# Performance work log

Hardware: AMD Instinct MI355X
Metric: run time of the kernel (lower is better)

The kernel has to match this reference:

```python
import jax, jax.numpy as jnp
import numpy as np

B, N, M, C, K = 4, 16384, 512, 256, 24
EPS = 1e-5


def setup_inputs() -> dict:
    key = jax.random.key(0)
    ks = jax.random.split(key, 5)
    return {
        "x": jax.random.normal(ks[0], (B, N, C), jnp.float32),
        "coords": jax.random.normal(ks[1], (B, N, 3), jnp.float32),
        "anchors": jax.random.normal(ks[2], (B, M, 3), jnp.float32),
        "fc_w": jax.random.normal(ks[3], (C, C), jnp.float32) * 0.05,
        "fc_b": jax.random.normal(ks[4], (C,), jnp.float32) * 0.05,
        "bn_gamma": jnp.ones((C,), jnp.float32),
        "bn_beta": jnp.zeros((C,), jnp.float32),
    }


def _build_incidence(coords, anchors):
    # squared distances suffice for top-k ordering (monotone in cdist)
    d2 = (
        jnp.sum(coords * coords, -1)[:, :, None]
        + jnp.sum(anchors * anchors, -1)[:, None, :]
        - 2.0 * jnp.einsum("bnd,bmd->bnm", coords, anchors)
    )  # [B,N,M]
    k = min(K, anchors.shape[1])
    _, idx = jax.lax.top_k(-d2, k)  # [B,N,k] nearest anchors
    b = jnp.arange(coords.shape[0])[:, None, None]
    n = jnp.arange(coords.shape[1])[None, :, None]
    H = jnp.zeros(d2.shape, d2.dtype).at[b, n, idx].set(1.0)
    return jax.lax.stop_gradient(H)  # built under torch.no_grad()


def _hypconv(x, H, fc_w, fc_b):
    xf = x @ fc_w.T + fc_b  # [B,N,C]
    deg_e = jnp.sum(H, axis=1)  # [B,M]  hyperedge degrees
    inv_e = jnp.where(deg_e > 0, 1.0 / deg_e, 0.0)[..., None]
    E = jnp.einsum("bnm,bnc->bmc", H, xf) * inv_e  # v -> e mean agg
    deg_v = jnp.sum(H, axis=2)  # [B,N]  node degrees
    inv_v = jnp.where(deg_v > 0, 1.0 / deg_v, 0.0)[..., None]
    return jnp.einsum("bnm,bmc->bnc", H, E) * inv_v  # e -> v mean agg


def reference(x, coords, anchors, fc_w, fc_b, bn_gamma, bn_beta):
    H = _build_incidence(coords, anchors)
    x = _hypconv(x, H, fc_w, fc_b) + x  # residual, [B,N,C]
    x = jnp.transpose(x, (0, 2, 1))  # [B,C,N]
    # BatchNorm1d (training-mode batch stats) over (B, N) per channel
    mean = jnp.mean(x, axis=(0, 2), keepdims=True)
    var = jnp.var(x, axis=(0, 2), keepdims=True)
    y = (x - mean) * jax.lax.rsqrt(var + EPS)
    y = y * bn_gamma[None, :, None] + bn_beta[None, :, None]
    return y * jax.nn.sigmoid(y)  # SiLU
```

## Files before the change

### kernel.cpp

```cpp
#include <hip/hip_runtime.h>

#define BB 4
#define NN 16384
#define MM 512
#define CCH 256
#define KNN 24
#define EPSV 1e-5f

typedef unsigned short ushort_t;

__device__ __forceinline__ unsigned int pk_bf16(float a, float b) {
    unsigned int ua = __float_as_uint(a), ub = __float_as_uint(b);
    ua += 0x7FFFu + ((ua >> 16) & 1u);
    ub += 0x7FFFu + ((ub >> 16) & 1u);
    return (ua >> 16) | (ub & 0xFFFF0000u);
}
__device__ __forceinline__ float lo_bf(unsigned int u) { return __uint_as_float(u << 16); }
__device__ __forceinline__ float hi_bf(unsigned int u) { return __uint_as_float(u & 0xFFFF0000u); }

__global__ __launch_bounds__(256) void k_cvt(const float* __restrict__ x,
                                             unsigned int* __restrict__ xh) {
    int i = blockIdx.x * 256 + threadIdx.x;
    float2 v = ((const float2*)x)[i];
    xh[i] = pk_bf16(v.x, v.y);
}

__global__ __launch_bounds__(256) void k_wt(const float* __restrict__ W, float* __restrict__ Wt) {
    int i = blockIdx.x * 256 + threadIdx.x;
    int co = i >> 8, ci = i & 255;
    Wt[(ci << 8) + co] = W[i];
}

#define AE(K) "v_max_u32 v89, v88, " K "\n\tv_min_u32 " K ", v88, " K "\n\t"
#define AO(K) "v_max_u32 v88, v89, " K "\n\tv_min_u32 " K ", v89, " K "\n\t"
#define BE(K) "v_max_u32 v91, v90, " K "\n\tv_min_u32 " K ", v90, " K "\n\t"
#define BO(K) "v_max_u32 v90, v91, " K "\n\tv_min_u32 " K ", v91, " K "\n\t"
#define CE(K) "v_max_u32 v93, v92, " K "\n\tv_min_u32 " K ", v92, " K "\n\t"
#define CO(K) "v_max_u32 v92, v93, " K "\n\tv_min_u32 " K ", v93, " K "\n\t"
#define DE(K) "v_max_u32 v95, v94, " K "\n\tv_min_u32 " K ", v94, " K "\n\t"
#define DO_(K) "v_max_u32 v94, v95, " K "\n\tv_min_u32 " K ", v95, " K "\n\t"
#define CHAIN4 \
    AE("v64") \
    AO("v65") BE("v64") \
    AE("v66") BO("v65") CE("v64") \
    AO("v67") BE("v66") CO("v65") DE("v64") \
    AE("v68") BO("v67") CE("v66") DO_("v65") \
    AO("v69") BE("v68") CO("v67") DE("v66") \
    AE("v70") BO("v69") CE("v68") DO_("v67") \
    AO("v71") BE("v70") CO("v69") DE("v68") \
    AE("v72") BO("v71") CE("v70") DO_("v69") \
    AO("v73") BE("v72") CO("v71") DE("v70") \
    AE("v74") BO("v73") CE("v72") DO_("v71") \
    AO("v75") BE("v74") CO("v73") DE("v72") \
    AE("v76") BO("v75") CE("v74") DO_("v73") \
    AO("v77") BE("v76") CO("v75") DE("v74") \
    AE("v78") BO("v77") CE("v76") DO_("v75") \
    AO("v79") BE("v78") CO("v77") DE("v76") \
    AE("v80") BO("v79") CE("v78") DO_("v77") \
    AO("v81") BE("v80") CO("v79") DE("v78") \
    AE("v82") BO("v81") CE("v80") DO_("v79") \
    AO("v83") BE("v82") CO("v81") DE("v80") \
    AE("v84") BO("v83") CE("v82") DO_("v81") \
    AO("v85") BE("v84") CO("v83") DE("v82") \
    AE("v86") BO("v85") CE("v84") DO_("v83") \
    AO("v87") BE("v86") CO("v85") DE("v84") \
              BO("v87") CE("v86") DO_("v85") \
                        CO("v87") DE("v86") \
                                  DO_("v87")
#define MRG(MI, KJ, K23MJ, K12PJ, K11MJ) \
    { unsigned int sA_ = (unsigned int)__shfl_xor((int)(K23MJ), 32); \
      unsigned int sB_ = (unsigned int)__shfl_xor((int)(K12PJ), 32); \
      MI = ((half == 0) ? min((KJ), sA_) : min(sB_, (K11MJ))) & 511u; }
__global__ __launch_bounds__(128, 2) void k_topk(const float* __restrict__ coords,
                                                 const float* __restrict__ anchors,
                                                 ushort_t* __restrict__ idx_out,
                                                 int* __restrict__ histT) {
    __shared__ float4 alds[MM];
    __shared__ int    hist[MM];
    int tid = threadIdx.x;
    int blk = blockIdx.x;
    int b  = blk >> 8;
    int g  = blk & 255;
    int n0 = g << 6;
    int lane = tid & 63;
    int half = lane >> 5;
    int n = n0 + ((tid >> 6) << 5) + (lane & 31);

    for (int m = tid; m < MM; m += 128) {
        float x_ = anchors[(b * MM + m) * 3 + 0];
        float y_ = anchors[(b * MM + m) * 3 + 1];
        float z_ = anchors[(b * MM + m) * 3 + 2];
        alds[m] = make_float4(x_, y_, z_, x_ * x_ + y_ * y_ + z_ * z_);
        hist[m] = 0;
    }
    __syncthreads();

    float cx = coords[(b * NN + n) * 3 + 0];
    float cy = coords[(b * NN + n) * 3 + 1];
    float cz = coords[(b * NN + n) * 3 + 2];
    float cn2 = cx * cx + cy * cy + cz * cz;

    unsigned int k0 = 0xFFFFFFFFu, k1 = 0xFFFFFFFFu, k2 = 0xFFFFFFFFu, k3 = 0xFFFFFFFFu,
                 k4 = 0xFFFFFFFFu, k5 = 0xFFFFFFFFu, k6 = 0xFFFFFFFFu, k7 = 0xFFFFFFFFu,
                 k8 = 0xFFFFFFFFu, k9 = 0xFFFFFFFFu, k10 = 0xFFFFFFFFu, k11 = 0xFFFFFFFFu,
                 k12 = 0xFFFFFFFFu, k13 = 0xFFFFFFFFu, k14 = 0xFFFFFFFFu, k15 = 0xFFFFFFFFu,
                 k16 = 0xFFFFFFFFu, k17 = 0xFFFFFFFFu, k18 = 0xFFFFFFFFu, k19 = 0xFFFFFFFFu,
                 k20 = 0xFFFFFFFFu, k21 = 0xFFFFFFFFu, k22 = 0xFFFFFFFFu, k23 = 0xFFFFFFFFu;

    int base = half << 8;
    float4 a0 = alds[base + 0];
    float4 a1 = alds[base + 1];
    float4 a2 = alds[base + 2];
    float4 a3 = alds[base + 3];
    float4 a4 = alds[base + 4];
    float4 a5 = alds[base + 5];
    float4 a6 = alds[base + 6];
    float4 a7 = alds[base + 7];
    for (int mm = 0; mm < 32; ++mm) {
        int nxt = (8 * mm + 8) & 255;
        float4 p0 = alds[base + nxt + 0];
        float4 p1 = alds[base + nxt + 1];
        float4 p2 = alds[base + nxt + 2];
        float4 p3 = alds[base + nxt + 3];
        float4 p4 = alds[base + nxt + 4];
        float4 p5 = alds[base + nxt + 5];
        float4 p6 = alds[base + nxt + 6];
        float4 p7 = alds[base + nxt + 7];
        float cd0 = cn2 + a0.w - 2.0f * (cx * a0.x + cy * a0.y + cz * a0.z);
        float cd1 = cn2 + a1.w - 2.0f * (cx * a1.x + cy * a1.y + cz * a1.z);
        float cd2 = cn2 + a2.w - 2.0f * (cx * a2.x + cy * a2.y + cz * a2.z);
        float cd3 = cn2 + a3.w - 2.0f * (cx * a3.x + cy * a3.y + cz * a3.z);
        float cd4 = cn2 + a4.w - 2.0f * (cx * a4.x + cy * a4.y + cz * a4.z);
        float cd5 = cn2 + a5.w - 2.0f * (cx * a5.x + cy * a5.y + cz * a5.z);
        float cd6 = cn2 + a6.w - 2.0f * (cx * a6.x + cy * a6.y + cz * a6.z);
        float cd7 = cn2 + a7.w - 2.0f * (cx * a7.x + cy * a7.y + cz * a7.z);
        int id0 = base + 8 * mm;
        unsigned int cA = ((__float_as_uint(cd0) ^ 0x80000000u) & 0xFFFFFE00u) | (unsigned)(id0 + 0);
        unsigned int cB = ((__float_as_uint(cd1) ^ 0x80000000u) & 0xFFFFFE00u) | (unsigned)(id0 + 1);
        unsigned int cC = ((__float_as_uint(cd2) ^ 0x80000000u) & 0xFFFFFE00u) | (unsigned)(id0 + 2);
        unsigned int cD = ((__float_as_uint(cd3) ^ 0x80000000u) & 0xFFFFFE00u) | (unsigned)(id0 + 3);
        unsigned int cE = ((__float_as_uint(cd4) ^ 0x80000000u) & 0xFFFFFE00u) | (unsigned)(id0 + 4);
        unsigned int cF = ((__float_as_uint(cd5) ^ 0x80000000u) & 0xFFFFFE00u) | (unsigned)(id0 + 5);
        unsigned int cG = ((__float_as_uint(cd6) ^ 0x80000000u) & 0xFFFFFE00u) | (unsigned)(id0 + 6);
        unsigned int cH = ((__float_as_uint(cd7) ^ 0x80000000u) & 0xFFFFFE00u) | (unsigned)(id0 + 7);
        asm volatile(
            CHAIN4
            "v_mov_b32 v88, v96\n\t"
            "v_mov_b32 v90, v98\n\t"
            "v_mov_b32 v92, v100\n\t"
            "v_mov_b32 v94, v102\n\t"
            CHAIN4
            : "+{v64}"(k0),  "+{v65}"(k1),  "+{v66}"(k2),  "+{v67}"(k3),
              "+{v68}"(k4),  "+{v69}"(k5),  "+{v70}"(k6),  "+{v71}"(k7),
              "+{v72}"(k8),  "+{v73}"(k9),  "+{v74}"(k10), "+{v75}"(k11),
              "+{v76}"(k12), "+{v77}"(k13), "+{v78}"(k14), "+{v79}"(k15),
              "+{v80}"(k16), "+{v81}"(k17), "+{v82}"(k18), "+{v83}"(k19),
              "+{v84}"(k20), "+{v85}"(k21), "+{v86}"(k22), "+{v87}"(k23),
              "+{v88}"(cA), "+{v90}"(cB), "+{v92}"(cC), "+{v94}"(cD),
              "+{v96}"(cE), "+{v98}"(cF), "+{v100}"(cG), "+{v102}"(cH)
            :
            : "v89", "v91", "v93", "v95");
        a0 = p0; a1 = p1; a2 = p2; a3 = p3;
        a4 = p4; a5 = p5; a6 = p6; a7 = p7;
    }

    unsigned int Mi0, Mi1, Mi2, Mi3, Mi4, Mi5, Mi6, Mi7, Mi8, Mi9, Mi10, Mi11;
    MRG(Mi0,  k0,  k23, k12, k11)
    MRG(Mi1,  k1,  k22, k13, k10)
    MRG(Mi2,  k2,  k21, k14, k9)
    MRG(Mi3,  k3,  k20, k15, k8)
    MRG(Mi4,  k4,  k19, k16, k7)
    MRG(Mi5,  k5,  k18, k17, k6)
    MRG(Mi6,  k6,  k17, k18, k5)
    MRG(Mi7,  k7,  k16, k19, k4)
    MRG(Mi8,  k8,  k15, k20, k3)
    MRG(Mi9,  k9,  k14, k21, k2)
    MRG(Mi10, k10, k13, k22, k1)
    MRG(Mi11, k11, k12, k23, k0)

    atomicAdd(&hist[Mi0], 1);  atomicAdd(&hist[Mi1], 1);
    atomicAdd(&hist[Mi2], 1);  atomicAdd(&hist[Mi3], 1);
    atomicAdd(&hist[Mi4], 1);  atomicAdd(&hist[Mi5], 1);
    atomicAdd(&hist[Mi6], 1);  atomicAdd(&hist[Mi7], 1);
    atomicAdd(&hist[Mi8], 1);  atomicAdd(&hist[Mi9], 1);
    atomicAdd(&hist[Mi10], 1); atomicAdd(&hist[Mi11], 1);

    unsigned int* ob = (unsigned int*)(idx_out + (size_t)(b * NN + n) * KNN + half * 12);
    ob[0] = Mi0 | (Mi1 << 16);
    ob[1] = Mi2 | (Mi3 << 16);
    ob[2] = Mi4 | (Mi5 << 16);
    ob[3] = Mi6 | (Mi7 << 16);
    ob[4] = Mi8 | (Mi9 << 16);
    ob[5] = Mi10 | (Mi11 << 16);

    __syncthreads();
    for (int m = tid; m < MM; m += 128)
        histT[((((b << 9) + m)) << 8) + g] = hist[m];
}

__global__ __launch_bounds__(64) void k_scan(const int* __restrict__ histT,
                                             int* __restrict__ posT,
                                             int* __restrict__ deg) {
    int e = blockIdx.x;
    int t = threadIdx.x;
    int4 v = ((const int4*)(histT + (e << 8)))[t];
    int s = v.x + v.y + v.z + v.w;
    int inc = s;
    #pragma unroll
    for (int off = 1; off < 64; off <<= 1) {
        int u = __shfl_up(inc, off);
        if (t >= off) inc += u;
    }
    int excl = inc - s;
    int4 o;
    o.x = excl; o.y = excl + v.x; o.z = o.y + v.y; o.w = o.z + v.z;
    ((int4*)(posT + (e << 8)))[t] = o;
    if (t == 63) deg[e] = inc;
}

__global__ __launch_bounds__(256) void k_offsets(const int* __restrict__ deg,
                                                 int* __restrict__ offs) {
    __shared__ int part[256];
    int t = threadIdx.x;
    int v[8];
    int s = 0;
    #pragma unroll
    for (int j = 0; j < 8; ++j) { v[j] = deg[t * 8 + j]; s += v[j]; }
    part[t] = s;
    __syncthreads();
    for (int off = 1; off < 256; off <<= 1) {
        int val = (t >= off) ? part[t - off] : 0;
        __syncthreads();
        part[t] += val;
        __syncthreads();
    }
    int excl = part[t] - s;
    #pragma unroll
    for (int j = 0; j < 8; ++j) { offs[t * 8 + j] = excl; excl += v[j]; }
}

__global__ __launch_bounds__(256) void k_fill2(const unsigned int* __restrict__ idxu,
                                               const int* __restrict__ posT,
                                               const int* __restrict__ offs,
                                               ushort_t* __restrict__ list) {
    __shared__ int pos[MM];
    __shared__ unsigned int ebuf[768];
    int tid = threadIdx.x;
    int blk = blockIdx.x;
    int b = blk >> 8, g = blk & 255;
    int n0 = g << 6;

    for (int m = tid; m < MM; m += 256) {
        int e = (b << 9) + m;
        pos[m] = offs[e] + posT[(e << 8) + g];
    }
    for (int i = tid; i < 768; i += 256)
        ebuf[i] = idxu[(size_t)(b * NN + n0) * 12 + i];
    __syncthreads();

    for (int i = tid; i < 768; i += 256) {
        unsigned int u = ebuf[i];
        int node = n0 + (i / 12);
        int p0 = atomicAdd(&pos[u & 0xFFFFu], 1);
        list[p0] = (ushort_t)node;
        int p1 = atomicAdd(&pos[u >> 16], 1);
        list[p1] = (ushort_t)node;
    }
}

__global__ __launch_bounds__(256) void k_edge2a(const unsigned int* __restrict__ xh,
                                                const ushort_t* __restrict__ list,
                                                const int* __restrict__ offs,
                                                const int* __restrict__ deg,
                                                float* __restrict__ S) {
    __shared__ ushort_t nl[256];
    __shared__ float red[8][64];
    int tid = threadIdx.x;
    int bi = blockIdx.x;
    int r = bi >> 12;
    int grp = (bi & 7) | (r << 3);
    int b = grp & 3;
    int q = grp >> 2;
    int e = (b << 9) | ((bi >> 3) & 511);
    int d = deg[e];
    int o = offs[e];
    int cp = tid & 31, rs = tid >> 5;
    const unsigned int* xb = xh + ((size_t)b << 21) + (q << 5);

    float l0 = 0.f, h0 = 0.f, l1 = 0.f, h1 = 0.f;
    for (int base2 = 0; base2 < d; base2 += 256) {
        int cnt = min(256, d - base2);
        if (tid < cnt) nl[tid] = list[(size_t)o + base2 + tid];
        __syncthreads();
        int i = 0;
        for (; i + 15 < cnt; i += 16) {
            unsigned int u0 = xb[((size_t)nl[i + rs] << 7) + cp];
            unsigned int u1 = xb[((size_t)nl[i + 8 + rs] << 7) + cp];
            l0 += lo_bf(u0); h0 += hi_bf(u0);
            l1 += lo_bf(u1); h1 += hi_bf(u1);
        }
        for (; i + 7 < cnt; i += 8) {
            unsigned int u = xb[((size_t)nl[i + rs] << 7) + cp];
            l0 += lo_bf(u); h0 += hi_bf(u);
        }
        if (i + rs < cnt) {
            unsigned int u = xb[((size_t)nl[i + rs] << 7) + cp];
            l1 += lo_bf(u); h1 += hi_bf(u);
        }
        __syncthreads();
    }
    red[rs][2 * cp] = l0 + l1;
    red[rs][2 * cp + 1] = h0 + h1;
    __syncthreads();
    if (tid < 64) {
        float s = 0.f;
        #pragma unroll
        for (int j = 0; j < 8; ++j) s += red[j][tid];
        S[((size_t)e << 8) + (q << 6) + tid] = s;
    }
}

__global__ __launch_bounds__(256) void k_edge2b(const float* __restrict__ S,
                                                const int* __restrict__ deg,
                                                const float* __restrict__ Wt,
                                                const float* __restrict__ fcb,
                                                unsigned int* __restrict__ Eph) {
    __shared__ float srow[CCH];
    __shared__ float rrow[CCH];
    int tid = threadIdx.x;
    int e = blockIdx.x;
    int d = deg[e];
    float inv = (d > 0) ? (1.0f / (float)d) : 0.0f;
    srow[tid] = S[((size_t)e << 8) + tid] * inv;
    __syncthreads();

    float c0 = (d > 0) ? fcb[tid] : 0.0f;
    float c1 = 0.f, c2 = 0.f, c3 = 0.f;
    #pragma unroll 4
    for (int ci = 0; ci < CCH; ci += 4) {
        c0 = fmaf(srow[ci + 0], Wt[((ci + 0) << 8) + tid], c0);
        c1 = fmaf(srow[ci + 1], Wt[((ci + 1) << 8) + tid], c1);
        c2 = fmaf(srow[ci + 2], Wt[((ci + 2) << 8) + tid], c2);
        c3 = fmaf(srow[ci + 3], Wt[((ci + 3) << 8) + tid], c3);
    }
    rrow[tid] = ((c0 + c1) + (c2 + c3)) * (1.0f / 24.0f);
    __syncthreads();
    if (tid < 128) Eph[((size_t)e << 7) + tid] = pk_bf16(rrow[2 * tid], rrow[2 * tid + 1]);
}

__global__ __launch_bounds__(256) void k_gather(const float* __restrict__ x,
                                                const unsigned int* __restrict__ idxu,
                                                const unsigned int* __restrict__ Eph,
                                                float* __restrict__ out,
                                                float* __restrict__ bn1,
                                                float* __restrict__ bn2) {
    __shared__ int   it[32 * KNN];
    __shared__ float tile[32][CCH + 1];
    int tid = threadIdx.x;
    int blk = blockIdx.x;
    int b = blk >> 9;
    int n0 = (blk & 511) << 5;
    int cp = tid & 127, rs = tid >> 7;

    for (int i = tid; i < 32 * 12; i += 256) {
        unsigned int u = idxu[(size_t)(b * NN + n0) * 12 + i];
        it[2 * i] = u & 0xFFFF;
        it[2 * i + 1] = u >> 16;
    }
    __syncthreads();

    const unsigned int* Eb = Eph + ((size_t)(b * MM) << 7);
    for (int j2 = 0; j2 < 16; ++j2) {
        int j = 2 * j2 + rs;
        int n = n0 + j;
        const int* itj = &it[j * KNN];
        float al = 0.f, ah = 0.f, bl = 0.f, bh = 0.f;
        float cl = 0.f, ch = 0.f, dl = 0.f, dh = 0.f;
        #pragma unroll
        for (int k = 0; k < KNN; k += 4) {
            unsigned int u0 = Eb[((size_t)itj[k + 0] << 7) + cp];
            unsigned int u1 = Eb[((size_t)itj[k + 1] << 7) + cp];
            unsigned int u2 = Eb[((size_t)itj[k + 2] << 7) + cp];
            unsigned int u3 = Eb[((size_t)itj[k + 3] << 7) + cp];
            al += lo_bf(u0); ah += hi_bf(u0);
            bl += lo_bf(u1); bh += hi_bf(u1);
            cl += lo_bf(u2); ch += hi_bf(u2);
            dl += lo_bf(u3); dh += hi_bf(u3);
        }
        float2 xv = ((const float2*)(x + (((size_t)(b * NN + n)) << 8)))[cp];
        tile[j][2 * cp + 0] = xv.x + ((al + bl) + (cl + dl));
        tile[j][2 * cp + 1] = xv.y + ((ah + bh) + (ch + dh));
    }
    __syncthreads();

    float sum = 0.f, ss = 0.f;
    #pragma unroll 4
    for (int j = 0; j < 32; ++j) {
        float v = tile[j][tid];
        sum += v; ss += v * v;
    }
    bn1[(size_t)blk * 256 + tid] = sum;
    bn2[(size_t)blk * 256 + tid] = ss;

    for (int i = tid; i < CCH * 32; i += 256) {
        int c2 = i >> 5, j2 = i & 31;
        out[(((size_t)(b * CCH + c2)) << 14) + n0 + j2] = tile[j2][c2];
    }
}

__global__ __launch_bounds__(256) void k_stats(const float* __restrict__ bn1,
                                               const float* __restrict__ bn2,
                                               const float* __restrict__ gamma,
                                               const float* __restrict__ beta,
                                               float* __restrict__ ab) {
    __shared__ float r1[256], r2[256];
    int c = blockIdx.x;
    int t = threadIdx.x;
    float s1 = 0.f, s2 = 0.f;
    for (int i = t; i < 2048; i += 256) {
        s1 += bn1[i * 256 + c];
        s2 += bn2[i * 256 + c];
    }
    r1[t] = s1; r2[t] = s2;
    __syncthreads();
    for (int o = 128; o > 0; o >>= 1) {
        if (t < o) { r1[t] += r1[t + o]; r2[t] += r2[t + o]; }
        __syncthreads();
    }
    if (t == 0) {
        float mean = r1[0] * (1.0f / 65536.0f);
        float var  = r2[0] * (1.0f / 65536.0f) - mean * mean;
        float istd = rsqrtf(var + EPSV);
        float a = gamma[c] * istd;
        ab[c] = a;
        ab[CCH + c] = beta[c] - mean * a;
    }
}

__global__ __launch_bounds__(256) void k_silu(float* __restrict__ out,
                                              const float* __restrict__ ab) {
    int i = blockIdx.x * 256 + threadIdx.x;
    int c = (i >> 12) & 255;
    float a = ab[c], bb = ab[CCH + c];
    float4 v = ((float4*)out)[i];
    float t0 = a * v.x + bb;
    float t1 = a * v.y + bb;
    float t2 = a * v.z + bb;
    float t3 = a * v.w + bb;
    v.x = t0 / (1.0f + __expf(-t0));
    v.y = t1 / (1.0f + __expf(-t1));
    v.z = t2 / (1.0f + __expf(-t2));
    v.w = t3 / (1.0f + __expf(-t3));
    ((float4*)out)[i] = v;
}

extern "C" void kernel_launch(void* const* d_in, const int* in_sizes, int n_in,
                              void* d_out, int out_size, void* d_ws, size_t ws_size,
                              hipStream_t stream) {
    (void)in_sizes; (void)n_in; (void)out_size; (void)ws_size;
    const float* x       = (const float*)d_in[0];
    const float* coords  = (const float*)d_in[1];
    const float* anchors = (const float*)d_in[2];
    const float* fcw     = (const float*)d_in[3];
    const float* fcb     = (const float*)d_in[4];
    const float* gamma   = (const float*)d_in[5];
    const float* beta    = (const float*)d_in[6];
    float* out = (float*)d_out;

    unsigned int* xh = (unsigned int*)d_out;

    char* ws = (char*)d_ws;
    ushort_t*     ws_idx   = (ushort_t*)    (ws + 0);
    int*          ws_deg   = (int*)         (ws + 3145728);
    int*          ws_offs  = (int*)         (ws + 3153920);
    ushort_t*     ws_list  = (ushort_t*)    (ws + 3162112);
    int*          ws_histT = (int*)         (ws + 6307840);
    int*          ws_posT  = (int*)         (ws + 8404992);
    unsigned int* ws_eph   = (unsigned int*)(ws + 10502144);
    float*        ws_S     = (float*)       (ws + 11550720);
    float*        ws_wt    = (float*)       (ws + 13647872);
    float*        ws_bn1   = (float*)       (ws + 13910016);
    float*        ws_bn2   = (float*)       (ws + 16007168);
    float*        ws_ab    = (float*)       (ws + 18104320);

    hipLaunchKernelGGL(k_cvt,     dim3(32768), dim3(256), 0, stream, x, xh);
    hipLaunchKernelGGL(k_wt,      dim3(256),   dim3(256), 0, stream, fcw, ws_wt);
    hipLaunchKernelGGL(k_topk,    dim3(1024),  dim3(128), 0, stream, coords, anchors, ws_idx, ws_histT);
    hipLaunchKernelGGL(k_scan,    dim3(2048),  dim3(64),  0, stream, ws_histT, ws_posT, ws_deg);
    hipLaunchKernelGGL(k_offsets, dim3(1),     dim3(256), 0, stream, ws_deg, ws_offs);
    hipLaunchKernelGGL(k_fill2,   dim3(1024),  dim3(256), 0, stream, (const unsigned int*)ws_idx, ws_posT, ws_offs, ws_list);
    hipLaunchKernelGGL(k_edge2a,  dim3(8192),  dim3(256), 0, stream, xh, ws_list, ws_offs, ws_deg, ws_S);
    hipLaunchKernelGGL(k_edge2b,  dim3(2048),  dim3(256), 0, stream, ws_S, ws_deg, ws_wt, fcb, ws_eph);
    hipLaunchKernelGGL(k_gather,  dim3(2048),  dim3(256), 0, stream, x, (const unsigned int*)ws_idx, ws_eph, out, ws_bn1, ws_bn2);
    hipLaunchKernelGGL(k_stats,   dim3(256),   dim3(256), 0, stream, ws_bn1, ws_bn2, gamma, beta, ws_ab);
    hipLaunchKernelGGL(k_silu,    dim3(16384), dim3(256), 0, stream, out, ws_ab);
}
```

Measured before the change: 293.6 us.

## Split top-k anchor scan four ways per point with shuffle-based bitonic merge

The top-k kernel now assigns each point to four lanes (quarters of the anchor set, 128 anchors each) instead of two, doubling block size to 256 threads. Each lane runs half as many insertion-chain iterations. Partial top-24 lists are merged via a cross-lane shuffle at distance 16 plus a bitonic clean-up network, then the existing distance-32 merge. This shortens the serial per-thread chain and raises thread-level parallelism, at the cost of extra merge work and higher register pressure with 256-thread blocks.

```diff
diff --git a/kernel.cpp b/kernel.cpp
--- a/kernel.cpp
+++ b/kernel.cpp
@@ -67,11 +67,12 @@
               BO("v87") CE("v86") DO_("v85") \
                         CO("v87") DE("v86") \
                                   DO_("v87")
+#define CEU(A, B) { unsigned int lo_ = min(A, B); B = max(A, B); A = lo_; }
 #define MRG(MI, KJ, K23MJ, K12PJ, K11MJ) \
     { unsigned int sA_ = (unsigned int)__shfl_xor((int)(K23MJ), 32); \
       unsigned int sB_ = (unsigned int)__shfl_xor((int)(K12PJ), 32); \
       MI = ((half == 0) ? min((KJ), sA_) : min(sB_, (K11MJ))) & 511u; }
-__global__ __launch_bounds__(128, 2) void k_topk(const float* __restrict__ coords,
+__global__ __launch_bounds__(256, 2) void k_topk(const float* __restrict__ coords,
                                                  const float* __restrict__ anchors,
                                                  ushort_t* __restrict__ idx_out,
                                                  int* __restrict__ histT) {
@@ -83,10 +84,13 @@
     int g  = blk & 255;
     int n0 = g << 6;
     int lane = tid & 63;
+    int w = tid >> 6;
+    int q = (lane >> 4) & 3;
     int half = lane >> 5;
-    int n = n0 + ((tid >> 6) << 5) + (lane & 31);
-
-    for (int m = tid; m < MM; m += 128) {
+    bool qa = ((lane >> 4) & 1) == 0;
+    int n = n0 + (w << 4) + (lane & 15);
+
+    for (int m = tid; m < MM; m += 256) {
         float x_ = anchors[(b * MM + m) * 3 + 0];
         float y_ = anchors[(b * MM + m) * 3 + 1];
         float z_ = anchors[(b * MM + m) * 3 + 2];
@@ -107,25 +111,25 @@
                  k16 = 0xFFFFFFFFu, k17 = 0xFFFFFFFFu, k18 = 0xFFFFFFFFu, k19 = 0xFFFFFFFFu,
                  k20 = 0xFFFFFFFFu, k21 = 0xFFFFFFFFu, k22 = 0xFFFFFFFFu, k23 = 0xFFFFFFFFu;
 
-    int base = half << 8;
-    float4 a0 = alds[base + 0];
-    float4 a1 = alds[base + 1];
-    float4 a2 = alds[base + 2];
-    float4 a3 = alds[base + 3];
-    float4 a4 = alds[base + 4];
-    float4 a5 = alds[base + 5];
-    float4 a6 = alds[base + 6];
-    float4 a7 = alds[base + 7];
-    for (int mm = 0; mm < 32; ++mm) {
-        int nxt = (8 * mm + 8) & 255;
-        float4 p0 = alds[base + nxt + 0];
-        float4 p1 = alds[base + nxt + 1];
-        float4 p2 = alds[base + nxt + 2];
-        float4 p3 = alds[base + nxt + 3];
-        float4 p4 = alds[base + nxt + 4];
-        float4 p5 = alds[base + nxt + 5];
-        float4 p6 = alds[base + nxt + 6];
-        float4 p7 = alds[base + nxt + 7];
+    int qbase = q << 7;
+    float4 a0 = alds[qbase + 0];
+    float4 a1 = alds[qbase + 1];
+    float4 a2 = alds[qbase + 2];
+    float4 a3 = alds[qbase + 3];
+    float4 a4 = alds[qbase + 4];
+    float4 a5 = alds[qbase + 5];
+    float4 a6 = alds[qbase + 6];
+    float4 a7 = alds[qbase + 7];
+    for (int mm = 0; mm < 16; ++mm) {
+        int nxt = (8 * mm + 8) & 127;
+        float4 p0 = alds[qbase + nxt + 0];
+        float4 p1 = alds[qbase + nxt + 1];
+        float4 p2 = alds[qbase + nxt + 2];
+        float4 p3 = alds[qbase + nxt + 3];
+        float4 p4 = alds[qbase + nxt + 4];
+        float4 p5 = alds[qbase + nxt + 5];
+        float4 p6 = alds[qbase + nxt + 6];
+        float4 p7 = alds[qbase + nxt + 7];
         float cd0 = cn2 + a0.w - 2.0f * (cx * a0.x + cy * a0.y + cz * a0.z);
         float cd1 = cn2 + a1.w - 2.0f * (cx * a1.x + cy * a1.y + cz * a1.z);
         float cd2 = cn2 + a2.w - 2.0f * (cx * a2.x + cy * a2.y + cz * a2.z);
@@ -134,7 +138,7 @@
         float cd5 = cn2 + a5.w - 2.0f * (cx * a5.x + cy * a5.y + cz * a5.z);
         float cd6 = cn2 + a6.w - 2.0f * (cx * a6.x + cy * a6.y + cz * a6.z);
         float cd7 = cn2 + a7.w - 2.0f * (cx * a7.x + cy * a7.y + cz * a7.z);
-        int id0 = base + 8 * mm;
+        int id0 = qbase + 8 * mm;
         unsigned int cA = ((__float_as_uint(cd0) ^ 0x80000000u) & 0xFFFFFE00u) | (unsigned)(id0 + 0);
         unsigned int cB = ((__float_as_uint(cd1) ^ 0x80000000u) & 0xFFFFFE00u) | (unsigned)(id0 + 1);
         unsigned int cC = ((__float_as_uint(cd2) ^ 0x80000000u) & 0xFFFFFE00u) | (unsigned)(id0 + 2);
@@ -164,37 +168,101 @@
         a4 = p4; a5 = p5; a6 = p6; a7 = p7;
     }
 
+    unsigned int r0  = (unsigned)__shfl_xor((int)k0, 16);
+    unsigned int r1  = (unsigned)__shfl_xor((int)k1, 16);
+    unsigned int r2  = (unsigned)__shfl_xor((int)k2, 16);
+    unsigned int r3  = (unsigned)__shfl_xor((int)k3, 16);
+    unsigned int r4  = (unsigned)__shfl_xor((int)k4, 16);
+    unsigned int r5  = (unsigned)__shfl_xor((int)k5, 16);
+    unsigned int r6  = (unsigned)__shfl_xor((int)k6, 16);
+    unsigned int r7  = (unsigned)__shfl_xor((int)k7, 16);
+    unsigned int r8  = (unsigned)__shfl_xor((int)k8, 16);
+    unsigned int r9  = (unsigned)__shfl_xor((int)k9, 16);
+    unsigned int r10 = (unsigned)__shfl_xor((int)k10, 16);
+    unsigned int r11 = (unsigned)__shfl_xor((int)k11, 16);
+    unsigned int r12 = (unsigned)__shfl_xor((int)k12, 16);
+    unsigned int r13 = (unsigned)__shfl_xor((int)k13, 16);
+    unsigned int r14 = (unsigned)__shfl_xor((int)k14, 16);
+    unsigned int r15 = (unsigned)__shfl_xor((int)k15, 16);
+    unsigned int r16_ = (unsigned)__shfl_xor((int)k16, 16);
+    unsigned int r17 = (unsigned)__shfl_xor((int)k17, 16);
+    unsigned int r18 = (unsigned)__shfl_xor((int)k18, 16);
+    unsigned int r19 = (unsigned)__shfl_xor((int)k19, 16);
+    unsigned int r20 = (unsigned)__shfl_xor((int)k20, 16);
+    unsigned int r21 = (unsigned)__shfl_xor((int)k21, 16);
+    unsigned int r22 = (unsigned)__shfl_xor((int)k22, 16);
+    unsigned int r23 = (unsigned)__shfl_xor((int)k23, 16);
+    unsigned int L0  = qa ? min(k0,  r23) : min(r0,  k23);
+    unsigned int L1  = qa ? min(k1,  r22) : min(r1,  k22);
+    unsigned int L2  = qa ? min(k2,  r21) : min(r2,  k21);
+    unsigned int L3  = qa ? min(k3,  r20) : min(r3,  k20);
+    unsigned int L4  = qa ? min(k4,  r19) : min(r4,  k19);
+    unsigned int L5  = qa ? min(k5,  r18) : min(r5,  k18);
+    unsigned int L6  = qa ? min(k6,  r17) : min(r6,  k17);
+    unsigned int L7  = qa ? min(k7,  r16_) : min(r7,  k16);
+    unsigned int L8  = qa ? min(k8,  r15) : min(r8,  k15);
+    unsigned int L9  = qa ? min(k9,  r14) : min(r9,  k14);
+    unsigned int L10 = qa ? min(k10, r13) : min(r10, k13);
+    unsigned int L11 = qa ? min(k11, r12) : min(r11, k12);
+    unsigned int L12 = qa ? min(k12, r11) : min(r12, k11);
+    unsigned int L13 = qa ? min(k13, r10) : min(r13, k10);
+    unsigned int L14 = qa ? min(k14, r9)  : min(r14, k9);
+    unsigned int L15 = qa ? min(k15, r8)  : min(r15, k8);
+    unsigned int L16 = qa ? min(k16, r7)  : min(r16_, k7);
+    unsigned int L17 = qa ? min(k17, r6)  : min(r17, k6);
+    unsigned int L18 = qa ? min(k18, r5)  : min(r18, k5);
+    unsigned int L19 = qa ? min(k19, r4)  : min(r19, k4);
+    unsigned int L20 = qa ? min(k20, r3)  : min(r20, k3);
+    unsigned int L21 = qa ? min(k21, r2)  : min(r21, k2);
+    unsigned int L22 = qa ? min(k22, r1)  : min(r22, k1);
+    unsigned int L23 = qa ? min(k23, r0)  : min(r23, k0);
+    CEU(L0, L16) CEU(L1, L17) CEU(L2, L18) CEU(L3, L19)
+    CEU(L4, L20) CEU(L5, L21) CEU(L6, L22) CEU(L7, L23)
+    CEU(L8, L16) CEU(L9, L17) CEU(L10, L18) CEU(L11, L19)
+    CEU(L12, L20) CEU(L13, L21) CEU(L14, L22) CEU(L15, L23)
+    CEU(L0, L4) CEU(L1, L5) CEU(L2, L6) CEU(L3, L7)
+    CEU(L8, L12) CEU(L9, L13) CEU(L10, L14) CEU(L11, L15)
+    CEU(L16, L20) CEU(L17, L21) CEU(L18, L22) CEU(L19, L23)
+    CEU(L0, L2) CEU(L1, L3) CEU(L4, L6) CEU(L5, L7)
+    CEU(L8, L10) CEU(L9, L11) CEU(L12, L14) CEU(L13, L15)
+    CEU(L16, L18) CEU(L17, L19) CEU(L20, L22) CEU(L21, L23)
+    CEU(L0, L1) CEU(L2, L3) CEU(L4, L5) CEU(L6, L7)
+    CEU(L8, L9) CEU(L10, L11) CEU(L12, L13) CEU(L14, L15)
+    CEU(L16, L17) CEU(L18, L19) CEU(L20, L21) CEU(L22, L23)
+
     unsigned int Mi0, Mi1, Mi2, Mi3, Mi4, Mi5, Mi6, Mi7, Mi8, Mi9, Mi10, Mi11;
-    MRG(Mi0,  k0,  k23, k12, k11)
-    MRG(Mi1,  k1,  k22, k13, k10)
-    MRG(Mi2,  k2,  k21, k14, k9)
-    MRG(Mi3,  k3,  k20, k15, k8)
-    MRG(Mi4,  k4,  k19, k16, k7)
-    MRG(Mi5,  k5,  k18, k17, k6)
-    MRG(Mi6,  k6,  k17, k18, k5)
-    MRG(Mi7,  k7,  k16, k19, k4)
-    MRG(Mi8,  k8,  k15, k20, k3)
-    MRG(Mi9,  k9,  k14, k21, k2)
-    MRG(Mi10, k10, k13, k22, k1)
-    MRG(Mi11, k11, k12, k23, k0)
-
-    atomicAdd(&hist[Mi0], 1);  atomicAdd(&hist[Mi1], 1);
-    atomicAdd(&hist[Mi2], 1);  atomicAdd(&hist[Mi3], 1);
-    atomicAdd(&hist[Mi4], 1);  atomicAdd(&hist[Mi5], 1);
-    atomicAdd(&hist[Mi6], 1);  atomicAdd(&hist[Mi7], 1);
-    atomicAdd(&hist[Mi8], 1);  atomicAdd(&hist[Mi9], 1);
-    atomicAdd(&hist[Mi10], 1); atomicAdd(&hist[Mi11], 1);
-
-    unsigned int* ob = (unsigned int*)(idx_out + (size_t)(b * NN + n) * KNN + half * 12);
-    ob[0] = Mi0 | (Mi1 << 16);
-    ob[1] = Mi2 | (Mi3 << 16);
-    ob[2] = Mi4 | (Mi5 << 16);
-    ob[3] = Mi6 | (Mi7 << 16);
-    ob[4] = Mi8 | (Mi9 << 16);
-    ob[5] = Mi10 | (Mi11 << 16);
-
-    __syncthreads();
-    for (int m = tid; m < MM; m += 128)
+    MRG(Mi0,  L0,  L23, L12, L11)
+    MRG(Mi1,  L1,  L22, L13, L10)
+    MRG(Mi2,  L2,  L21, L14, L9)
+    MRG(Mi3,  L3,  L20, L15, L8)
+    MRG(Mi4,  L4,  L19, L16, L7)
+    MRG(Mi5,  L5,  L18, L17, L6)
+    MRG(Mi6,  L6,  L17, L18, L5)
+    MRG(Mi7,  L7,  L16, L19, L4)
+    MRG(Mi8,  L8,  L15, L20, L3)
+    MRG(Mi9,  L9,  L14, L21, L2)
+    MRG(Mi10, L10, L13, L22, L1)
+    MRG(Mi11, L11, L12, L23, L0)
+
+    if (qa) {
+        atomicAdd(&hist[Mi0], 1);  atomicAdd(&hist[Mi1], 1);
+        atomicAdd(&hist[Mi2], 1);  atomicAdd(&hist[Mi3], 1);
+        atomicAdd(&hist[Mi4], 1);  atomicAdd(&hist[Mi5], 1);
+        atomicAdd(&hist[Mi6], 1);  atomicAdd(&hist[Mi7], 1);
+        atomicAdd(&hist[Mi8], 1);  atomicAdd(&hist[Mi9], 1);
+        atomicAdd(&hist[Mi10], 1); atomicAdd(&hist[Mi11], 1);
+
+        unsigned int* ob = (unsigned int*)(idx_out + (size_t)(b * NN + n) * KNN + half * 12);
+        ob[0] = Mi0 | (Mi1 << 16);
+        ob[1] = Mi2 | (Mi3 << 16);
+        ob[2] = Mi4 | (Mi5 << 16);
+        ob[3] = Mi6 | (Mi7 << 16);
+        ob[4] = Mi8 | (Mi9 << 16);
+        ob[5] = Mi10 | (Mi11 << 16);
+    }
+
+    __syncthreads();
+    for (int m = tid; m < MM; m += 256)
         histT[((((b << 9) + m)) << 8) + g] = hist[m];
 }
 
@@ -485,7 +553,7 @@
 
     hipLaunchKernelGGL(k_cvt,     dim3(32768), dim3(256), 0, stream, x, xh);
     hipLaunchKernelGGL(k_wt,      dim3(256),   dim3(256), 0, stream, fcw, ws_wt);
-    hipLaunchKernelGGL(k_topk,    dim3(1024),  dim3(128), 0, stream, coords, anchors, ws_idx, ws_histT);
+    hipLaunchKernelGGL(k_topk,    dim3(1024),  dim3(256), 0, stream, coords, anchors, ws_idx, ws_histT);
     hipLaunchKernelGGL(k_scan,    dim3(2048),  dim3(64),  0, stream, ws_histT, ws_posT, ws_deg);
     hipLaunchKernelGGL(k_offsets, dim3(1),     dim3(256), 0, stream, ws_deg, ws_offs);
     hipLaunchKernelGGL(k_fill2,   dim3(1024),  dim3(256), 0, stream, (const unsigned int*)ws_idx, ws_posT, ws_offs, ws_list);
```

Result: faster. 270.4 us (-7.9%).
